# Optimization experiments

Measured on AMD Instinct MI355X. Metric: run time of the kernel, lower is better.

Reference implementation:

```python
import jax, jax.numpy as jnp
import numpy as np

H = 20  # hidden size (hardcoded in the torch module)

def setup_inputs() -> dict:
    key = jax.random.key(0)
    ks = jax.random.split(key, 7)
    s = 0.1  # keep activations in a sane range for tanh/sigmoid
    return {
        "x":     jax.random.normal(ks[0], (8192, 512, 12), dtype=jnp.float32),
        "w_ih":  jax.random.normal(ks[1], (4 * H, 12), dtype=jnp.float32) * s,
        "w_hh":  jax.random.normal(ks[2], (4 * H, H), dtype=jnp.float32) * s,
        "b_ih":  jax.random.normal(ks[3], (4 * H,), dtype=jnp.float32) * s,
        "b_hh":  jax.random.normal(ks[4], (4 * H,), dtype=jnp.float32) * s,
        "w_out": jax.random.normal(ks[5], (10, H), dtype=jnp.float32) * s,
        "b_out": jax.random.normal(ks[6], (10,), dtype=jnp.float32) * s,
    }

def reference(x, w_ih, w_hh, b_ih, b_hh, w_out, b_out):
    # x: [B, T, I]. Single-layer LSTM (PyTorch gate order i,f,g,o), zero init state,
    # then Linear on the last hidden state.
    B, T, _ = x.shape
    # Precompute input projections for all timesteps: [T, B, 4H]
    x_proj = jnp.einsum('bti,gi->tbg', x, w_ih) + (b_ih + b_hh)

    def step(carry, xt):
        h, c = carry                      # each [B, H]
        gates = xt + h @ w_hh.T           # [B, 4H]
        i, f, g, o = jnp.split(gates, 4, axis=-1)
        i = jax.nn.sigmoid(i)
        f = jax.nn.sigmoid(f)
        g = jnp.tanh(g)
        o = jax.nn.sigmoid(o)
        c = f * c + i * g
        h = o * jnp.tanh(c)
        return (h, c), None

    h0 = jnp.zeros((B, H), dtype=x.dtype)
    c0 = jnp.zeros((B, H), dtype=x.dtype)
    (h_last, _), _ = jax.lax.scan(step, (h0, c0), x_proj)
    # out = Linear(h_T): r_out[:, -1, :] == h_n for a single-layer LSTM
    return h_last @ w_out.T + b_out
```

## Files before the change

### kernel.cpp

```cpp
#include <hip/hip_runtime.h>

typedef _Float16 f16;
typedef f16 f16x4 __attribute__((ext_vector_type(4)));
typedef f16 f16x8 __attribute__((ext_vector_type(8)));
typedef float f32x4 __attribute__((ext_vector_type(4)));

#define T_STEPS 512
#define INPUT   12
#define HID     20
#define KDIM    32
#define BSTRIDE 40
#define BATCH   16
#define NTILES  5

static __device__ __forceinline__ void lds_fence() {
    asm volatile("s_waitcnt lgkmcnt(0)" ::: "memory");
}

__global__ __launch_bounds__(64) void lstm_kernel(
    const float* __restrict__ x,
    const float* __restrict__ w_ih,
    const float* __restrict__ w_hh,
    const float* __restrict__ b_ih,
    const float* __restrict__ b_hh,
    const float* __restrict__ w_out,
    const float* __restrict__ b_out,
    float* __restrict__ out)
{
    __shared__ __align__(16) f16 Wc[80][KDIM];
    __shared__ __align__(16) f16 Bbuf[2][BATCH][BSTRIDE];

    const int lane = threadIdx.x;
    const int b    = lane & 15;
    const int quad = lane >> 4;

    for (int i = lane; i < 80 * KDIM; i += 64) {
        int n = i >> 5, k = i & 31;
        int g = n & 3;
        int u = 4 * (n >> 4) + ((n >> 2) & 3);
        int row = g * HID + u;
        float v = (k < INPUT) ? w_ih[row * INPUT + k] : w_hh[row * HID + (k - INPUT)];
        float sc = (g == 2) ? 2.8853900817779268f : -1.4426950408889634f;
        Wc[n][k] = (f16)(v * sc);
    }

    f32x4 cbias[NTILES];
#pragma unroll
    for (int w = 0; w < NTILES; ++w) {
        int u = 4 * w + quad;
#pragma unroll
        for (int g = 0; g < 4; ++g) {
            float sc = (g == 2) ? 2.8853900817779268f : -1.4426950408889634f;
            cbias[w][g] = sc * (b_ih[g * HID + u] + b_hh[g * HID + u]);
        }
    }

#pragma unroll
    for (int w = 0; w < NTILES; ++w)
        Bbuf[0][b][INPUT + 4 * w + quad] = (f16)0.f;

    const bool xload = quad < 3;
    const float* xptr = x + (size_t)(blockIdx.x * BATCH + b) * (T_STEPS * INPUT) + 4 * quad;

    f32x4 q0 = {0.f,0.f,0.f,0.f}, q1 = q0, q2 = q0, q3 = q0;
    if (xload) {
        f32x4 x0 = *(const f32x4*)xptr;
        f16x4 xc;
#pragma unroll
        for (int j = 0; j < 4; ++j) xc[j] = (f16)x0[j];
        *(f16x4*)&Bbuf[0][b][4 * quad] = xc;
        q0 = *(const f32x4*)(xptr + 1 * INPUT);
        q1 = *(const f32x4*)(xptr + 2 * INPUT);
        q2 = *(const f32x4*)(xptr + 3 * INPUT);
        q3 = *(const f32x4*)(xptr + 4 * INPUT);
    }

    lds_fence();

    f16x8 afrag[NTILES];
#pragma unroll
    for (int w = 0; w < NTILES; ++w)
        afrag[w] = *(const f16x8*)&Wc[16 * w + b][quad * 8];

    float cc[NTILES] = {0.f, 0.f, 0.f, 0.f, 0.f};

    auto step = [&](int pj, f32x4& qreg, int tload) {
        lds_fence();
        f16x8 bfrag = *(const f16x8*)&Bbuf[pj][b][quad * 8];

        if (xload) {
            f16x4 xc;
#pragma unroll
            for (int j = 0; j < 4; ++j) xc[j] = (f16)qreg[j];
            *(f16x4*)&Bbuf[pj ^ 1][b][4 * quad] = xc;
            int tl = tload < T_STEPS ? tload : T_STEPS - 1;
            qreg = *(const f32x4*)(xptr + (size_t)tl * INPUT);
        }

        f32x4 acc[NTILES];
#pragma unroll
        for (int w = 0; w < NTILES; ++w)
            acc[w] = __builtin_amdgcn_mfma_f32_16x16x32_f16(afrag[w], bfrag, cbias[w], 0, 0, 0);

#pragma unroll
        for (int w = 0; w < NTILES; ++w) {
            float ei = __builtin_amdgcn_exp2f(acc[w][0]);
            float ef = __builtin_amdgcn_exp2f(acc[w][1]);
            float eg = __builtin_amdgcn_exp2f(acc[w][2]);
            float eo = __builtin_amdgcn_exp2f(acc[w][3]);
            float Ai = 1.f + ei, Af = 1.f + ef, Ag = 1.f + eg, Ao = 1.f + eo;
            float P  = Ai * Ag;
            float rD = __builtin_amdgcn_rcpf(P * Af);
            float nm = __builtin_fmaf(eg - 1.f, Af, cc[w] * P);
            float c  = nm * rD;
            cc[w] = c;
            float et = __builtin_amdgcn_exp2f(2.8853900817779268f * c);
            float At = 1.f + et;
            float rM = __builtin_amdgcn_rcpf(At * Ao);
            float h  = (et - 1.f) * rM;
            Bbuf[pj ^ 1][b][INPUT + 4 * w + quad] = (f16)h;
        }
    };

#pragma unroll 1
    for (int t4 = 0; t4 < T_STEPS; t4 += 4) {
        step(0, q0, t4 + 5);
        step(1, q1, t4 + 6);
        step(0, q2, t4 + 7);
        step(1, q3, t4 + 8);
    }

    lds_fence();

    for (int i = lane; i < BATCH * 10; i += 64) {
        int ob = i / 10, oo = i - 10 * ob;
        float s = b_out[oo];
#pragma unroll
        for (int u2 = 0; u2 < HID; ++u2)
            s += w_out[oo * HID + u2] * (float)Bbuf[0][ob][INPUT + u2];
        out[(size_t)(blockIdx.x * BATCH + ob) * 10 + oo] = s;
    }
}

extern "C" void kernel_launch(void* const* d_in, const int* in_sizes, int n_in,
                              void* d_out, int out_size, void* d_ws, size_t ws_size,
                              hipStream_t stream) {
    const float* x     = (const float*)d_in[0];
    const float* w_ih  = (const float*)d_in[1];
    const float* w_hh  = (const float*)d_in[2];
    const float* b_ih  = (const float*)d_in[3];
    const float* b_hh  = (const float*)d_in[4];
    const float* w_out = (const float*)d_in[5];
    const float* b_out = (const float*)d_in[6];
    float* out = (float*)d_out;

    const int blocks = 8192 / BATCH;
    hipLaunchKernelGGL(lstm_kernel, dim3(blocks), dim3(64), 0, stream,
                       x, w_ih, w_hh, b_ih, b_hh, w_out, b_out, out);
}
```

Measured before the change: 468.7 us.

## Interleave two independent batch groups per wavefront to overlap recurrent dependency chains

Each wavefront now processes two 16-sequence groups, issuing MFMAs and gate math for both so the latency of one group's serial recurrence is hidden by the other's work. The grid shrinks to half as many blocks and LDS state is duplicated per group. This trades cross-wave parallelism for in-wave ILP and raises register pressure, which could lower occupancy.

```diff
diff --git a/kernel.cpp b/kernel.cpp
--- a/kernel.cpp
+++ b/kernel.cpp
@@ -12,6 +12,7 @@
 #define BSTRIDE 40
 #define BATCH   16
 #define NTILES  5
+#define NGRP    2
 
 static __device__ __forceinline__ void lds_fence() {
     asm volatile("s_waitcnt lgkmcnt(0)" ::: "memory");
@@ -28,7 +29,7 @@
     float* __restrict__ out)
 {
     __shared__ __align__(16) f16 Wc[80][KDIM];
-    __shared__ __align__(16) f16 Bbuf[2][BATCH][BSTRIDE];
+    __shared__ __align__(16) f16 Bbuf[NGRP][2][BATCH][BSTRIDE];
 
     const int lane = threadIdx.x;
     const int b    = lane & 15;
@@ -56,23 +57,34 @@
     }
 
 #pragma unroll
-    for (int w = 0; w < NTILES; ++w)
-        Bbuf[0][b][INPUT + 4 * w + quad] = (f16)0.f;
+    for (int g = 0; g < NGRP; ++g)
+#pragma unroll
+        for (int w = 0; w < NTILES; ++w)
+            Bbuf[g][0][b][INPUT + 4 * w + quad] = (f16)0.f;
 
     const bool xload = quad < 3;
-    const float* xptr = x + (size_t)(blockIdx.x * BATCH + b) * (T_STEPS * INPUT) + 4 * quad;
+    const float* xp0 = x + (size_t)(blockIdx.x * (BATCH * NGRP) + 0 * BATCH + b) * (T_STEPS * INPUT) + 4 * quad;
+    const float* xp1 = x + (size_t)(blockIdx.x * (BATCH * NGRP) + 1 * BATCH + b) * (T_STEPS * INPUT) + 4 * quad;
 
-    f32x4 q0 = {0.f,0.f,0.f,0.f}, q1 = q0, q2 = q0, q3 = q0;
+    f32x4 z4 = {0.f, 0.f, 0.f, 0.f};
+    f32x4 q00 = z4, q01 = z4, q02 = z4, q03 = z4;
+    f32x4 q10 = z4, q11 = z4, q12 = z4, q13 = z4;
     if (xload) {
-        f32x4 x0 = *(const f32x4*)xptr;
-        f16x4 xc;
+        f32x4 xa = *(const f32x4*)xp0;
+        f32x4 xb = *(const f32x4*)xp1;
+        f16x4 xc0, xc1;
 #pragma unroll
-        for (int j = 0; j < 4; ++j) xc[j] = (f16)x0[j];
-        *(f16x4*)&Bbuf[0][b][4 * quad] = xc;
-        q0 = *(const f32x4*)(xptr + 1 * INPUT);
-        q1 = *(const f32x4*)(xptr + 2 * INPUT);
-        q2 = *(const f32x4*)(xptr + 3 * INPUT);
-        q3 = *(const f32x4*)(xptr + 4 * INPUT);
+        for (int j = 0; j < 4; ++j) { xc0[j] = (f16)xa[j]; xc1[j] = (f16)xb[j]; }
+        *(f16x4*)&Bbuf[0][0][b][4 * quad] = xc0;
+        *(f16x4*)&Bbuf[1][0][b][4 * quad] = xc1;
+        q00 = *(const f32x4*)(xp0 + 1 * INPUT);
+        q01 = *(const f32x4*)(xp0 + 2 * INPUT);
+        q02 = *(const f32x4*)(xp0 + 3 * INPUT);
+        q03 = *(const f32x4*)(xp0 + 4 * INPUT);
+        q10 = *(const f32x4*)(xp1 + 1 * INPUT);
+        q11 = *(const f32x4*)(xp1 + 2 * INPUT);
+        q12 = *(const f32x4*)(xp1 + 3 * INPUT);
+        q13 = *(const f32x4*)(xp1 + 4 * INPUT);
     }
 
     lds_fence();
@@ -82,63 +94,89 @@
     for (int w = 0; w < NTILES; ++w)
         afrag[w] = *(const f16x8*)&Wc[16 * w + b][quad * 8];
 
-    float cc[NTILES] = {0.f, 0.f, 0.f, 0.f, 0.f};
+    float cc0[NTILES] = {0.f, 0.f, 0.f, 0.f, 0.f};
+    float cc1[NTILES] = {0.f, 0.f, 0.f, 0.f, 0.f};
 
-    auto step = [&](int pj, f32x4& qreg, int tload) {
+    auto dual_step = [&](int pj, f32x4& qA, f32x4& qB, int tload) {
         lds_fence();
-        f16x8 bfrag = *(const f16x8*)&Bbuf[pj][b][quad * 8];
+        f16x8 bf0 = *(const f16x8*)&Bbuf[0][pj][b][quad * 8];
+        f16x8 bf1 = *(const f16x8*)&Bbuf[1][pj][b][quad * 8];
 
         if (xload) {
-            f16x4 xc;
+            f16x4 xc0, xc1;
 #pragma unroll
-            for (int j = 0; j < 4; ++j) xc[j] = (f16)qreg[j];
-            *(f16x4*)&Bbuf[pj ^ 1][b][4 * quad] = xc;
+            for (int j = 0; j < 4; ++j) { xc0[j] = (f16)qA[j]; xc1[j] = (f16)qB[j]; }
+            *(f16x4*)&Bbuf[0][pj ^ 1][b][4 * quad] = xc0;
+            *(f16x4*)&Bbuf[1][pj ^ 1][b][4 * quad] = xc1;
             int tl = tload < T_STEPS ? tload : T_STEPS - 1;
-            qreg = *(const f32x4*)(xptr + (size_t)tl * INPUT);
+            qA = *(const f32x4*)(xp0 + (size_t)tl * INPUT);
+            qB = *(const f32x4*)(xp1 + (size_t)tl * INPUT);
         }
 
-        f32x4 acc[NTILES];
+        f32x4 acc0[NTILES], acc1[NTILES];
 #pragma unroll
-        for (int w = 0; w < NTILES; ++w)
-            acc[w] = __builtin_amdgcn_mfma_f32_16x16x32_f16(afrag[w], bfrag, cbias[w], 0, 0, 0);
+        for (int w = 0; w < NTILES; ++w) {
+            acc0[w] = __builtin_amdgcn_mfma_f32_16x16x32_f16(afrag[w], bf0, cbias[w], 0, 0, 0);
+            acc1[w] = __builtin_amdgcn_mfma_f32_16x16x32_f16(afrag[w], bf1, cbias[w], 0, 0, 0);
+        }
 
 #pragma unroll
         for (int w = 0; w < NTILES; ++w) {
-            float ei = __builtin_amdgcn_exp2f(acc[w][0]);
-            float ef = __builtin_amdgcn_exp2f(acc[w][1]);
-            float eg = __builtin_amdgcn_exp2f(acc[w][2]);
-            float eo = __builtin_amdgcn_exp2f(acc[w][3]);
-            float Ai = 1.f + ei, Af = 1.f + ef, Ag = 1.f + eg, Ao = 1.f + eo;
-            float P  = Ai * Ag;
-            float rD = __builtin_amdgcn_rcpf(P * Af);
-            float nm = __builtin_fmaf(eg - 1.f, Af, cc[w] * P);
-            float c  = nm * rD;
-            cc[w] = c;
-            float et = __builtin_amdgcn_exp2f(2.8853900817779268f * c);
-            float At = 1.f + et;
-            float rM = __builtin_amdgcn_rcpf(At * Ao);
-            float h  = (et - 1.f) * rM;
-            Bbuf[pj ^ 1][b][INPUT + 4 * w + quad] = (f16)h;
+            {
+                float ei = __builtin_amdgcn_exp2f(acc0[w][0]);
+                float ef = __builtin_amdgcn_exp2f(acc0[w][1]);
+                float eg = __builtin_amdgcn_exp2f(acc0[w][2]);
+                float eo = __builtin_amdgcn_exp2f(acc0[w][3]);
+                float Ai = 1.f + ei, Af = 1.f + ef, Ag = 1.f + eg, Ao = 1.f + eo;
+                float P  = Ai * Ag;
+                float rD = __builtin_amdgcn_rcpf(P * Af);
+                float nm = __builtin_fmaf(eg - 1.f, Af, cc0[w] * P);
+                float c  = nm * rD;
+                cc0[w] = c;
+                float et = __builtin_amdgcn_exp2f(2.8853900817779268f * c);
+                float At = 1.f + et;
+                float rM = __builtin_amdgcn_rcpf(At * Ao);
+                float h  = (et - 1.f) * rM;
+                Bbuf[0][pj ^ 1][b][INPUT + 4 * w + quad] = (f16)h;
+            }
+            {
+                float ei = __builtin_amdgcn_exp2f(acc1[w][0]);
+                float ef = __builtin_amdgcn_exp2f(acc1[w][1]);
+                float eg = __builtin_amdgcn_exp2f(acc1[w][2]);
+                float eo = __builtin_amdgcn_exp2f(acc1[w][3]);
+                float Ai = 1.f + ei, Af = 1.f + ef, Ag = 1.f + eg, Ao = 1.f + eo;
+                float P  = Ai * Ag;
+                float rD = __builtin_amdgcn_rcpf(P * Af);
+                float nm = __builtin_fmaf(eg - 1.f, Af, cc1[w] * P);
+                float c  = nm * rD;
+                cc1[w] = c;
+                float et = __builtin_amdgcn_exp2f(2.8853900817779268f * c);
+                float At = 1.f + et;
+                float rM = __builtin_amdgcn_rcpf(At * Ao);
+                float h  = (et - 1.f) * rM;
+                Bbuf[1][pj ^ 1][b][INPUT + 4 * w + quad] = (f16)h;
+            }
         }
     };
 
 #pragma unroll 1
     for (int t4 = 0; t4 < T_STEPS; t4 += 4) {
-        step(0, q0, t4 + 5);
-        step(1, q1, t4 + 6);
-        step(0, q2, t4 + 7);
-        step(1, q3, t4 + 8);
+        dual_step(0, q00, q10, t4 + 5);
+        dual_step(1, q01, q11, t4 + 6);
+        dual_step(0, q02, q12, t4 + 7);
+        dual_step(1, q03, q13, t4 + 8);
     }
 
     lds_fence();
 
-    for (int i = lane; i < BATCH * 10; i += 64) {
-        int ob = i / 10, oo = i - 10 * ob;
+    for (int i = lane; i < BATCH * NGRP * 10; i += 64) {
+        int bb = i / 10, oo = i - 10 * bb;
+        int g  = bb >> 4, ob = bb & 15;
         float s = b_out[oo];
 #pragma unroll
         for (int u2 = 0; u2 < HID; ++u2)
-            s += w_out[oo * HID + u2] * (float)Bbuf[0][ob][INPUT + u2];
-        out[(size_t)(blockIdx.x * BATCH + ob) * 10 + oo] = s;
+            s += w_out[oo * HID + u2] * (float)Bbuf[g][0][ob][INPUT + u2];
+        out[(size_t)(blockIdx.x * (BATCH * NGRP) + bb) * 10 + oo] = s;
     }
 }
 
@@ -154,7 +192,7 @@
     const float* b_out = (const float*)d_in[6];
     float* out = (float*)d_out;
 
-    const int blocks = 8192 / BATCH;
+    const int blocks = 8192 / (BATCH * NGRP);
     hipLaunchKernelGGL(lstm_kernel, dim3(blocks), dim3(64), 0, stream,
                        x, w_ih, w_hh, b_ih, b_hh, w_out, b_out, out);
 }
```

Measured after the change: 607.3 us. 1.3x slower.

## Keep LSTM hidden state in registers and build B-fragment via ds_bpermute

Applied to the files above, without the earlier changes.

Remaps which hidden units each lane owns so that most of the next step's MFMA B-operand comes straight from the lane's own registers. The few missing values are fetched with cross-lane ds_bpermute, replacing the per-step LDS double-buffer writes, waitcnt fence and fragment reload. This aims to shorten the serial recurrence latency. In exchange it adds permute and select instructions, and every lane now loads x with some redundant global reads. The output projection is also rewritten to use register partial sums reduced with xor shuffles.

```diff
diff --git a/kernel.cpp b/kernel.cpp
--- a/kernel.cpp
+++ b/kernel.cpp
@@ -1,20 +1,30 @@
 #include <hip/hip_runtime.h>
 
 typedef _Float16 f16;
-typedef f16 f16x4 __attribute__((ext_vector_type(4)));
 typedef f16 f16x8 __attribute__((ext_vector_type(8)));
 typedef float f32x4 __attribute__((ext_vector_type(4)));
+typedef unsigned int u32;
+typedef unsigned short u16;
 
 #define T_STEPS 512
 #define INPUT   12
 #define HID     20
 #define KDIM    32
-#define BSTRIDE 40
 #define BATCH   16
 #define NTILES  5
 
-static __device__ __forceinline__ void lds_fence() {
-    asm volatile("s_waitcnt lgkmcnt(0)" ::: "memory");
+static __device__ __forceinline__ f16 u16_as_f16(u16 v) {
+    union { u16 u; f16 h; } cv; cv.u = v; return cv.h;
+}
+static __device__ __forceinline__ u16 f16_as_u16(f16 h) {
+    union { u16 u; f16 h; } cv; cv.h = h; return cv.u;
+}
+
+static __device__ __forceinline__ int own_unit(int mq, int w) {
+    return (mq == 0) ? (w < 3 ? 9 + w : 14 + w)
+         : (mq == 1) ? (w < 4 ? w : 19)
+         : (mq == 2) ? (4 + w)
+         : (12 + w);
 }
 
 __global__ __launch_bounds__(64) void lstm_kernel(
@@ -27,80 +37,104 @@
     const float* __restrict__ b_out,
     float* __restrict__ out)
 {
-    __shared__ __align__(16) f16 Wc[80][KDIM];
-    __shared__ __align__(16) f16 Bbuf[2][BATCH][BSTRIDE];
+    __shared__ __align__(16) f16 Wc[NTILES][16][KDIM];
 
     const int lane = threadIdx.x;
-    const int b    = lane & 15;
-    const int quad = lane >> 4;
-
-    for (int i = lane; i < 80 * KDIM; i += 64) {
-        int n = i >> 5, k = i & 31;
-        int g = n & 3;
-        int u = 4 * (n >> 4) + ((n >> 2) & 3);
-        int row = g * HID + u;
+    const int c    = lane & 15;
+    const int q    = lane >> 4;
+
+    for (int i = lane; i < NTILES * 16 * KDIM; i += 64) {
+        int w  = i >> 9;
+        int m  = (i >> 5) & 15;
+        int k  = i & 31;
+        int mq = m >> 2, r = m & 3;
+        int u  = own_unit(mq, w);
+        int row = r * HID + u;
         float v = (k < INPUT) ? w_ih[row * INPUT + k] : w_hh[row * HID + (k - INPUT)];
-        float sc = (g == 2) ? 2.8853900817779268f : -1.4426950408889634f;
-        Wc[n][k] = (f16)(v * sc);
-    }
+        float sc = (r == 2) ? 2.8853900817779268f : -1.4426950408889634f;
+        Wc[w][m][k] = (f16)(v * sc);
+    }
+
+    int own[NTILES];
+#pragma unroll
+    for (int w = 0; w < NTILES; ++w) own[w] = own_unit(q, w);
 
     f32x4 cbias[NTILES];
 #pragma unroll
     for (int w = 0; w < NTILES; ++w) {
-        int u = 4 * w + quad;
-#pragma unroll
-        for (int g = 0; g < 4; ++g) {
-            float sc = (g == 2) ? 2.8853900817779268f : -1.4426950408889634f;
-            cbias[w][g] = sc * (b_ih[g * HID + u] + b_hh[g * HID + u]);
+#pragma unroll
+        for (int r = 0; r < 4; ++r) {
+            float sc = (r == 2) ? 2.8853900817779268f : -1.4426950408889634f;
+            cbias[w][r] = sc * (b_ih[r * HID + own[w]] + b_hh[r * HID + own[w]]);
         }
     }
 
+    const float* xbase = x + (size_t)(blockIdx.x * BATCH + c) * (T_STEPS * INPUT);
+    const float* xptrA = xbase + (q == 1 ? 8 : 0);
+    const float* xptrB = xbase + 4;
+
+    f16   h16[NTILES] = {(f16)0.f, (f16)0.f, (f16)0.f, (f16)0.f, (f16)0.f};
+    float cc[NTILES]  = {0.f, 0.f, 0.f, 0.f, 0.f};
+
+    const int idx0 = 4 * c;
+    const int idx1 = 4 * (16 + c);
+    auto assemble = [&](f32x4 xA, f32x4 xB) -> f16x8 {
+        u32 pk01 = (u32)f16_as_u16(h16[0]) | ((u32)f16_as_u16(h16[1]) << 16);
+        u32 pk23 = (u32)f16_as_u16(h16[2]) | ((u32)f16_as_u16(h16[3]) << 16);
+        u32 pk44 = (u32)f16_as_u16(h16[4]);
+        u32 P1 = (u32)__builtin_amdgcn_ds_bpermute(idx0, (int)pk01);
+        u32 P2 = (u32)__builtin_amdgcn_ds_bpermute(idx0, (int)pk23);
+        u32 P3 = (u32)__builtin_amdgcn_ds_bpermute(idx0, (int)pk44);
+        u32 P4 = (u32)__builtin_amdgcn_ds_bpermute(idx1, (int)pk44);
+
+        f16 xf[8];
+#pragma unroll
+        for (int j = 0; j < 4; ++j) { xf[j] = (f16)xA[j]; xf[4 + j] = (f16)xB[j]; }
+
+        const bool is0 = (q == 0), is1 = (q == 1), is2 = (q == 2), le1 = (q <= 1);
+        f16 hb[8];
+        hb[0] = le1 ? xf[0] : h16[0];
+        hb[1] = le1 ? xf[1] : h16[1];
+        hb[2] = le1 ? xf[2] : h16[2];
+        hb[3] = le1 ? xf[3] : h16[3];
+        hb[4] = is0 ? xf[4] : (is1 ? h16[0] : h16[4]);
+        hb[5] = is0 ? xf[5] : (is1 ? h16[1] : (is2 ? u16_as_f16((u16)P1)
+                                                   : u16_as_f16((u16)(P2 >> 16))));
+        hb[6] = is0 ? xf[6] : (is1 ? h16[2] : (is2 ? u16_as_f16((u16)(P1 >> 16))
+                                                   : u16_as_f16((u16)P3)));
+        hb[7] = is0 ? xf[7] : (is1 ? h16[3] : (is2 ? u16_as_f16((u16)P2)
+                                                   : u16_as_f16((u16)P4)));
+        f16x8 r;
+#pragma unroll
+        for (int j = 0; j < 8; ++j) r[j] = hb[j];
+        return r;
+    };
+
+    f32x4 x0A = *(const f32x4*)xptrA;
+    f32x4 x0B = *(const f32x4*)xptrB;
+    f32x4 qA0 = *(const f32x4*)(xptrA + 1 * INPUT), qB0 = *(const f32x4*)(xptrB + 1 * INPUT);
+    f32x4 qA1 = *(const f32x4*)(xptrA + 2 * INPUT), qB1 = *(const f32x4*)(xptrB + 2 * INPUT);
+    f32x4 qA2 = *(const f32x4*)(xptrA + 3 * INPUT), qB2 = *(const f32x4*)(xptrB + 3 * INPUT);
+    f32x4 qA3 = *(const f32x4*)(xptrA + 4 * INPUT), qB3 = *(const f32x4*)(xptrB + 4 * INPUT);
+
+    asm volatile("s_waitcnt lgkmcnt(0)" ::: "memory");
+
+    f16x8 afrag[NTILES];
 #pragma unroll
     for (int w = 0; w < NTILES; ++w)
-        Bbuf[0][b][INPUT + 4 * w + quad] = (f16)0.f;
-
-    const bool xload = quad < 3;
-    const float* xptr = x + (size_t)(blockIdx.x * BATCH + b) * (T_STEPS * INPUT) + 4 * quad;
-
-    f32x4 q0 = {0.f,0.f,0.f,0.f}, q1 = q0, q2 = q0, q3 = q0;
-    if (xload) {
-        f32x4 x0 = *(const f32x4*)xptr;
-        f16x4 xc;
-#pragma unroll
-        for (int j = 0; j < 4; ++j) xc[j] = (f16)x0[j];
-        *(f16x4*)&Bbuf[0][b][4 * quad] = xc;
-        q0 = *(const f32x4*)(xptr + 1 * INPUT);
-        q1 = *(const f32x4*)(xptr + 2 * INPUT);
-        q2 = *(const f32x4*)(xptr + 3 * INPUT);
-        q3 = *(const f32x4*)(xptr + 4 * INPUT);
-    }
-
-    lds_fence();
-
-    f16x8 afrag[NTILES];
-#pragma unroll
-    for (int w = 0; w < NTILES; ++w)
-        afrag[w] = *(const f16x8*)&Wc[16 * w + b][quad * 8];
-
-    float cc[NTILES] = {0.f, 0.f, 0.f, 0.f, 0.f};
-
-    auto step = [&](int pj, f32x4& qreg, int tload) {
-        lds_fence();
-        f16x8 bfrag = *(const f16x8*)&Bbuf[pj][b][quad * 8];
-
-        if (xload) {
-            f16x4 xc;
-#pragma unroll
-            for (int j = 0; j < 4; ++j) xc[j] = (f16)qreg[j];
-            *(f16x4*)&Bbuf[pj ^ 1][b][4 * quad] = xc;
-            int tl = tload < T_STEPS ? tload : T_STEPS - 1;
-            qreg = *(const f32x4*)(xptr + (size_t)tl * INPUT);
-        }
-
+        afrag[w] = *(const f16x8*)&Wc[w][c][q * 8];
+
+    f16x8 bfrag = assemble(x0A, x0B);
+
+    auto step = [&](f32x4& sA, f32x4& sB, int tload) {
         f32x4 acc[NTILES];
 #pragma unroll
         for (int w = 0; w < NTILES; ++w)
             acc[w] = __builtin_amdgcn_mfma_f32_16x16x32_f16(afrag[w], bfrag, cbias[w], 0, 0, 0);
+
+        int tl = tload < T_STEPS ? tload : T_STEPS - 1;
+        f32x4 nA = *(const f32x4*)(xptrA + (size_t)tl * INPUT);
+        f32x4 nB = *(const f32x4*)(xptrB + (size_t)tl * INPUT);
 
 #pragma unroll
         for (int w = 0; w < NTILES; ++w) {
@@ -112,33 +146,46 @@
             float P  = Ai * Ag;
             float rD = __builtin_amdgcn_rcpf(P * Af);
             float nm = __builtin_fmaf(eg - 1.f, Af, cc[w] * P);
-            float c  = nm * rD;
-            cc[w] = c;
-            float et = __builtin_amdgcn_exp2f(2.8853900817779268f * c);
+            float cn = nm * rD;
+            cc[w] = cn;
+            float et = __builtin_amdgcn_exp2f(2.8853900817779268f * cn);
             float At = 1.f + et;
             float rM = __builtin_amdgcn_rcpf(At * Ao);
-            float h  = (et - 1.f) * rM;
-            Bbuf[pj ^ 1][b][INPUT + 4 * w + quad] = (f16)h;
+            h16[w] = (f16)((et - 1.f) * rM);
         }
+
+        bfrag = assemble(sA, sB);
+        sA = nA; sB = nB;
     };
 
 #pragma unroll 1
     for (int t4 = 0; t4 < T_STEPS; t4 += 4) {
-        step(0, q0, t4 + 5);
-        step(1, q1, t4 + 6);
-        step(0, q2, t4 + 7);
-        step(1, q3, t4 + 8);
-    }
-
-    lds_fence();
-
-    for (int i = lane; i < BATCH * 10; i += 64) {
-        int ob = i / 10, oo = i - 10 * ob;
-        float s = b_out[oo];
-#pragma unroll
-        for (int u2 = 0; u2 < HID; ++u2)
-            s += w_out[oo * HID + u2] * (float)Bbuf[0][ob][INPUT + u2];
-        out[(size_t)(blockIdx.x * BATCH + ob) * 10 + oo] = s;
+        step(qA0, qB0, t4 + 5);
+        step(qA1, qB1, t4 + 6);
+        step(qA2, qB2, t4 + 7);
+        step(qA3, qB3, t4 + 8);
+    }
+
+    float po[10];
+#pragma unroll
+    for (int o = 0; o < 10; ++o) {
+        float s = 0.f;
+#pragma unroll
+        for (int w = 0; w < NTILES; ++w)
+            s += w_out[o * HID + own[w]] * (float)h16[w];
+        po[o] = s;
+    }
+#pragma unroll
+    for (int o = 0; o < 10; ++o) {
+        po[o] += __shfl_xor(po[o], 16);
+        po[o] += __shfl_xor(po[o], 32);
+    }
+    if (q < 2) {
+#pragma unroll
+        for (int i = 0; i < 5; ++i) {
+            int o = 5 * q + i;
+            out[(size_t)(blockIdx.x * BATCH + c) * 10 + o] = po[o] + b_out[o];
+        }
     }
 }
 
```

Result: slower. 493.2 us (+5.2%).

## Split LSTM gate tiles across two wavefronts with per-step block barrier

Applied to the files above, without the earlier changes.

Each block now runs two wavefronts. The five MFMA gate tiles are divided 3/2 between them, and the x staging moves to the second wave. A workgroup barrier after every timestep keeps the hidden-state buffer consistent across the waves. The goal is to shorten the serial per-step critical path by running the gate math in parallel. The cost is an s_barrier on every step and an uneven split of work between the two waves.

```diff
diff --git a/kernel.cpp b/kernel.cpp
--- a/kernel.cpp
+++ b/kernel.cpp
@@ -11,13 +11,13 @@
 #define KDIM    32
 #define BSTRIDE 40
 #define BATCH   16
-#define NTILES  5
+#define BLOCK   128
 
-static __device__ __forceinline__ void lds_fence() {
-    asm volatile("s_waitcnt lgkmcnt(0)" ::: "memory");
+static __device__ __forceinline__ void block_barrier() {
+    asm volatile("s_waitcnt lgkmcnt(0)\n\ts_barrier" ::: "memory");
 }
 
-__global__ __launch_bounds__(64) void lstm_kernel(
+__global__ __launch_bounds__(BLOCK) void lstm_kernel(
     const float* __restrict__ x,
     const float* __restrict__ w_ih,
     const float* __restrict__ w_hh,
@@ -30,11 +30,13 @@
     __shared__ __align__(16) f16 Wc[80][KDIM];
     __shared__ __align__(16) f16 Bbuf[2][BATCH][BSTRIDE];
 
-    const int lane = threadIdx.x;
-    const int b    = lane & 15;
-    const int quad = lane >> 4;
+    const int tid  = threadIdx.x;
+    const int wid  = tid >> 6;
+    const int lane = tid & 63;
+    const int c    = lane & 15;
+    const int q    = lane >> 4;
 
-    for (int i = lane; i < 80 * KDIM; i += 64) {
+    for (int i = tid; i < 80 * KDIM; i += BLOCK) {
         int n = i >> 5, k = i & 31;
         int g = n & 3;
         int u = 4 * (n >> 4) + ((n >> 2) & 3);
@@ -44,95 +46,100 @@
         Wc[n][k] = (f16)(v * sc);
     }
 
-    f32x4 cbias[NTILES];
+    const int TBASE = wid ? 3 : 0;
+    const int TCNT  = wid ? 2 : 3;
+
+    int   uu[3]    = {0, 0, 0};
+    f32x4 cbias[3] = {};
+    float cc[3]    = {0.f, 0.f, 0.f};
 #pragma unroll
-    for (int w = 0; w < NTILES; ++w) {
-        int u = 4 * w + quad;
+    for (int j = 0; j < 3; ++j)
+        if (j < TCNT) {
+            uu[j] = 4 * (TBASE + j) + q;
 #pragma unroll
-        for (int g = 0; g < 4; ++g) {
-            float sc = (g == 2) ? 2.8853900817779268f : -1.4426950408889634f;
-            cbias[w][g] = sc * (b_ih[g * HID + u] + b_hh[g * HID + u]);
+            for (int r = 0; r < 4; ++r) {
+                float sc = (r == 2) ? 2.8853900817779268f : -1.4426950408889634f;
+                cbias[j][r] = sc * (b_ih[r * HID + uu[j]] + b_hh[r * HID + uu[j]]);
+            }
+            Bbuf[0][c][INPUT + uu[j]] = (f16)0.f;
         }
-    }
 
-#pragma unroll
-    for (int w = 0; w < NTILES; ++w)
-        Bbuf[0][b][INPUT + 4 * w + quad] = (f16)0.f;
+    const bool stage = (wid == 1) && (lane < 48);
+    const int  l3 = stage ? lane : 0;
+    const int  cb = l3 / 3, p = l3 - 3 * cb;
+    const float* xptr = x + (size_t)(blockIdx.x * BATCH + cb) * (T_STEPS * INPUT) + 4 * p;
 
-    const bool xload = quad < 3;
-    const float* xptr = x + (size_t)(blockIdx.x * BATCH + b) * (T_STEPS * INPUT) + 4 * quad;
-
-    f32x4 q0 = {0.f,0.f,0.f,0.f}, q1 = q0, q2 = q0, q3 = q0;
-    if (xload) {
+    f32x4 z4 = {0.f, 0.f, 0.f, 0.f};
+    f32x4 qq0 = z4, qq1 = z4, qq2 = z4, qq3 = z4;
+    if (stage) {
         f32x4 x0 = *(const f32x4*)xptr;
         f16x4 xc;
 #pragma unroll
-        for (int j = 0; j < 4; ++j) xc[j] = (f16)x0[j];
-        *(f16x4*)&Bbuf[0][b][4 * quad] = xc;
-        q0 = *(const f32x4*)(xptr + 1 * INPUT);
-        q1 = *(const f32x4*)(xptr + 2 * INPUT);
-        q2 = *(const f32x4*)(xptr + 3 * INPUT);
-        q3 = *(const f32x4*)(xptr + 4 * INPUT);
+        for (int jj = 0; jj < 4; ++jj) xc[jj] = (f16)x0[jj];
+        *(f16x4*)&Bbuf[0][cb][4 * p] = xc;
+        qq0 = *(const f32x4*)(xptr + 1 * INPUT);
+        qq1 = *(const f32x4*)(xptr + 2 * INPUT);
+        qq2 = *(const f32x4*)(xptr + 3 * INPUT);
+        qq3 = *(const f32x4*)(xptr + 4 * INPUT);
     }
+    __syncthreads();
 
-    lds_fence();
+    f16x8 afrag[3];
+#pragma unroll
+    for (int j = 0; j < 3; ++j)
+        if (j < TCNT)
+            afrag[j] = *(const f16x8*)&Wc[16 * (TBASE + j) + c][q * 8];
 
-    f16x8 afrag[NTILES];
-#pragma unroll
-    for (int w = 0; w < NTILES; ++w)
-        afrag[w] = *(const f16x8*)&Wc[16 * w + b][quad * 8];
+    auto step = [&](int pj, f32x4& qs, int tload) {
+        f16x8 bfrag = *(const f16x8*)&Bbuf[pj][c][q * 8];
 
-    float cc[NTILES] = {0.f, 0.f, 0.f, 0.f, 0.f};
-
-    auto step = [&](int pj, f32x4& qreg, int tload) {
-        lds_fence();
-        f16x8 bfrag = *(const f16x8*)&Bbuf[pj][b][quad * 8];
-
-        if (xload) {
+        if (stage) {
             f16x4 xc;
 #pragma unroll
-            for (int j = 0; j < 4; ++j) xc[j] = (f16)qreg[j];
-            *(f16x4*)&Bbuf[pj ^ 1][b][4 * quad] = xc;
+            for (int jj = 0; jj < 4; ++jj) xc[jj] = (f16)qs[jj];
+            *(f16x4*)&Bbuf[pj ^ 1][cb][4 * p] = xc;
             int tl = tload < T_STEPS ? tload : T_STEPS - 1;
-            qreg = *(const f32x4*)(xptr + (size_t)tl * INPUT);
+            qs = *(const f32x4*)(xptr + (size_t)tl * INPUT);
         }
 
-        f32x4 acc[NTILES];
+        f32x4 acc[3];
 #pragma unroll
-        for (int w = 0; w < NTILES; ++w)
-            acc[w] = __builtin_amdgcn_mfma_f32_16x16x32_f16(afrag[w], bfrag, cbias[w], 0, 0, 0);
+        for (int j = 0; j < 3; ++j)
+            if (j < TCNT)
+                acc[j] = __builtin_amdgcn_mfma_f32_16x16x32_f16(afrag[j], bfrag, cbias[j], 0, 0, 0);
 
 #pragma unroll
-        for (int w = 0; w < NTILES; ++w) {
-            float ei = __builtin_amdgcn_exp2f(acc[w][0]);
-            float ef = __builtin_amdgcn_exp2f(acc[w][1]);
-            float eg = __builtin_amdgcn_exp2f(acc[w][2]);
-            float eo = __builtin_amdgcn_exp2f(acc[w][3]);
-            float Ai = 1.f + ei, Af = 1.f + ef, Ag = 1.f + eg, Ao = 1.f + eo;
-            float P  = Ai * Ag;
-            float rD = __builtin_amdgcn_rcpf(P * Af);
-            float nm = __builtin_fmaf(eg - 1.f, Af, cc[w] * P);
-            float c  = nm * rD;
-            cc[w] = c;
-            float et = __builtin_amdgcn_exp2f(2.8853900817779268f * c);
-            float At = 1.f + et;
-            float rM = __builtin_amdgcn_rcpf(At * Ao);
-            float h  = (et - 1.f) * rM;
-            Bbuf[pj ^ 1][b][INPUT + 4 * w + quad] = (f16)h;
-        }
+        for (int j = 0; j < 3; ++j)
+            if (j < TCNT) {
+                float ei = __builtin_amdgcn_exp2f(acc[j][0]);
+                float ef = __builtin_amdgcn_exp2f(acc[j][1]);
+                float eg = __builtin_amdgcn_exp2f(acc[j][2]);
+                float eo = __builtin_amdgcn_exp2f(acc[j][3]);
+                float Ai = 1.f + ei, Af = 1.f + ef, Ag = 1.f + eg, Ao = 1.f + eo;
+                float P  = Ai * Ag;
+                float rD = __builtin_amdgcn_rcpf(P * Af);
+                float nm = __builtin_fmaf(eg - 1.f, Af, cc[j] * P);
+                float cn = nm * rD;
+                cc[j] = cn;
+                float et = __builtin_amdgcn_exp2f(2.8853900817779268f * cn);
+                float At = 1.f + et;
+                float rM = __builtin_amdgcn_rcpf(At * Ao);
+                float h  = (et - 1.f) * rM;
+                Bbuf[pj ^ 1][c][INPUT + uu[j]] = (f16)h;
+            }
+
+        block_barrier();
     };
 
 #pragma unroll 1
     for (int t4 = 0; t4 < T_STEPS; t4 += 4) {
-        step(0, q0, t4 + 5);
-        step(1, q1, t4 + 6);
-        step(0, q2, t4 + 7);
-        step(1, q3, t4 + 8);
+        step(0, qq0, t4 + 5);
+        step(1, qq1, t4 + 6);
+        step(0, qq2, t4 + 7);
+        step(1, qq3, t4 + 8);
     }
 
-    lds_fence();
-
-    for (int i = lane; i < BATCH * 10; i += 64) {
+    for (int i = tid; i < BATCH * 10; i += BLOCK) {
         int ob = i / 10, oo = i - 10 * ob;
         float s = b_out[oo];
 #pragma unroll
@@ -155,6 +162,6 @@
     float* out = (float*)d_out;
 
     const int blocks = 8192 / BATCH;
-    hipLaunchKernelGGL(lstm_kernel, dim3(blocks), dim3(64), 0, stream,
+    hipLaunchKernelGGL(lstm_kernel, dim3(blocks), dim3(BLOCK), 0, stream,
                        x, w_ih, w_hh, b_ih, b_hh, w_out, b_out, out);
 }
```

Measured after the change: 434.4 us. 1.08x faster.
